# Kernel tuning notes

Hardware: AMD Instinct MI355X
Metric: run time of the kernel (lower is better)

The kernel has to match this reference:

```python
import jax, jax.numpy as jnp
import numpy as np

N = 50000
NUM_USERS = 20000
E = 800000
IN_DIM = 256
OUT_DIM = 256
H = 8
DK = OUT_DIM // H


def setup_inputs() -> dict:
    key = jax.random.key(0)
    ks = jax.random.split(key, 16)
    inp = {
        "x": jax.random.normal(ks[0], (N, IN_DIM), dtype=jnp.float32),
        "row": jax.random.randint(ks[1], (E,), 0, N, dtype=jnp.int32),
        "col": jax.random.randint(ks[2], (E,), 0, N, dtype=jnp.int32),
        "relation_emb": jax.random.normal(ks[3], (OUT_DIM,), dtype=jnp.float32),
        "user_text_embs": jax.random.normal(ks[4], (NUM_USERS, IN_DIM), dtype=jnp.float32),
        "item_text_embs": jax.random.normal(ks[5], (N - NUM_USERS, IN_DIM), dtype=jnp.float32),
        "Wq": jax.random.normal(ks[6], (OUT_DIM, IN_DIM), dtype=jnp.float32) * 0.02,
        "bq": jnp.zeros((OUT_DIM,), dtype=jnp.float32),
        "Wk": jax.random.normal(ks[7], (OUT_DIM, IN_DIM), dtype=jnp.float32) * 0.02,
        "bk": jnp.zeros((OUT_DIM,), dtype=jnp.float32),
        "Wv": jax.random.normal(ks[8], (OUT_DIM, IN_DIM), dtype=jnp.float32) * 0.02,
        "bv": jnp.zeros((OUT_DIM,), dtype=jnp.float32),
        "Wo": jax.random.normal(ks[9], (OUT_DIM, OUT_DIM), dtype=jnp.float32) * 0.02,
        "bo": jnp.zeros((OUT_DIM,), dtype=jnp.float32),
    }
    return inp


def reference(x, row, col, relation_emb, user_text_embs, item_text_embs,
              Wq, bq, Wk, bk, Wv, bv, Wo, bo):
    # text_emb: users first, then items (matches torch zeros_like + slice assign)
    text_emb = jnp.concatenate([user_text_embs, item_text_embs], axis=0)  # [N, in_dim]

    Q = (text_emb @ Wq.T + bq).reshape(N, H, DK)
    K = (text_emb @ Wk.T + bk).reshape(N, H, DK)
    V = (x @ Wv.T + bv).reshape(N, H, DK)

    Q_ = Q[col]  # [E, H, DK]
    K_ = K[row]
    V_ = V[row]
    rel = relation_emb.reshape(1, H, DK)

    scores = jnp.sum(Q_ * (K_ + rel), axis=-1) / np.sqrt(DK).astype(np.float32)  # [E, H]

    # segment softmax over destination node (col)
    m = jax.ops.segment_max(scores, col, num_segments=N)          # [N, H]
    e = jnp.exp(scores - m[col])                                   # [E, H]
    denom = jax.ops.segment_sum(e, col, num_segments=N)           # [N, H]
    attn = e / denom[col]                                          # [E, H]

    out = jax.ops.segment_sum(attn[:, :, None] * V_, col, num_segments=N)  # [N, H, DK]
    out = out.reshape(N, OUT_DIM)
    return out @ Wo.T + bo
```

## Files before the change

### kernel.cpp

```cpp
#include <hip/hip_runtime.h>
#include <hip/hip_bf16.h>

#define N_NODES   50000
#define N_USERS   20000
#define N_EDGES   800000
#define DIM       256
#define NHEAD     8
#define DKH       32
#define NBLK_SCAN ((N_NODES + 255) / 256)
#define NGRP_PAD  3128
#define NBLK_HIST ((N_EDGES + 255) / 256)
#define NBLK_G64  (NGRP_PAD / 4)
#define KVROW     768

typedef __attribute__((ext_vector_type(8))) short bf16x8;
typedef __attribute__((ext_vector_type(4))) float f32x4;
typedef __attribute__((ext_vector_type(4))) unsigned short u16x4;
typedef __attribute__((ext_vector_type(8))) unsigned short u16x8;

__device__ inline unsigned short f2bf(float f) {
    union { __hip_bfloat16 b; unsigned short u; } cv;
    cv.b = __float2bfloat16(f);
    return cv.u;
}
__device__ inline float bf2f(unsigned short u) {
    return __uint_as_float(((unsigned int)u) << 16);
}
__device__ inline unsigned char f2fp8(float f) {
    unsigned int p = __builtin_amdgcn_cvt_pk_fp8_f32(f, f, 0, false);
    return (unsigned char)(p & 0xff);
}


__global__ void prep_kernel(const float* __restrict__ Wq, const float* __restrict__ Wk,
                            const float* __restrict__ Wv, const float* __restrict__ Wo,
                            unsigned short* __restrict__ Wb2,
                            const int* __restrict__ col, int* __restrict__ cnt,
                            int* __restrict__ erank)
{
    int b = blockIdx.x;
    if (b < 128) {
        int gid = b * 256 + threadIdx.x;
        const float* srcs[4] = { Wq, Wk, Wv, Wo };
        int m = gid >> 13, slot = gid & 8191;
        int lane = slot & 63, ks = (slot >> 6) & 7, g = slot >> 9;
        int c = g * 16 + (lane & 15);
        int d = ks * 32 + (lane >> 4) * 8;
        const float* s = srcs[m] + (size_t)c * DIM + d;
        float4 f0 = *(const float4*)s, f1 = *(const float4*)(s + 4);
        u16x8 o = { f2bf(f0.x), f2bf(f0.y), f2bf(f0.z), f2bf(f0.w),
                    f2bf(f1.x), f2bf(f1.y), f2bf(f1.z), f2bf(f1.w) };
        *(u16x8*)(Wb2 + (size_t)m * 65536 + (size_t)slot * 8) = o;
    } else {
        int e = (b - 128) * 256 + threadIdx.x;
        if (e < N_EDGES) erank[e] = atomicAdd(&cnt[col[e]], 1);
    }
}

__device__ __forceinline__ void stage_a_lds(const float* __restrict__ Alo,
                                            const float* __restrict__ Ahi,
                                            int split, int row0, int M,
                                            unsigned short* Asm, int tid)
{
    const int w = tid >> 6, lane = tid & 63;
    #pragma unroll
    for (int it = 0; it < 8; ++it) {
        int f = it * 4 + w;
        int g = f >> 3, ks = f & 7;
        int r = g * 16 + (lane & 15);
        int d = ks * 32 + (lane >> 4) * 8;
        int ga = row0 + r; if (ga >= M) ga = M - 1;
        const float* src = ((ga < split) ? Alo + (size_t)ga * DIM
                                         : Ahi + (size_t)(ga - split) * DIM) + d;
        float4 f0 = *(const float4*)src, f1 = *(const float4*)(src + 4);
        u16x8 hv = { f2bf(f0.x), f2bf(f0.y), f2bf(f0.z), f2bf(f0.w),
                     f2bf(f1.x), f2bf(f1.y), f2bf(f1.z), f2bf(f1.w) };
        *(u16x8*)((char*)Asm + (size_t)f * 1024 + lane * 16) = hv;
    }
}

__device__ __forceinline__ void mfma_core_lds(const unsigned short* Asm,
                                              const unsigned short* __restrict__ W2,
                                              f32x4 acc[2][8], int lane, int wid)
{
    const int gAl = (wid >> 1) * 2;
    const int gB = (wid & 1) * 8;
    #pragma unroll
    for (int ks = 0; ks < 8; ++ks) {
        bf16x8 a[2], b[8];
        #pragma unroll
        for (int i = 0; i < 2; ++i)
            a[i] = *(const bf16x8*)((const char*)Asm + (size_t)((gAl + i) * 8 + ks) * 1024 + lane * 16);
        #pragma unroll
        for (int j = 0; j < 8; ++j)
            b[j] = *(const bf16x8*)(W2 + (size_t)((gB + j) * 8 + ks) * 512 + lane * 8);
        #pragma unroll
        for (int i = 0; i < 2; ++i)
            #pragma unroll
            for (int j = 0; j < 8; ++j)
                acc[i][j] = __builtin_amdgcn_mfma_f32_16x16x32_bf16(a[i], b[j], acc[i][j], 0, 0, 0);
    }
}

__device__ __forceinline__ void mfma_core64(const unsigned short* __restrict__ A2,
                                            const unsigned short* __restrict__ W2,
                                            int row0, f32x4 acc[2][8],
                                            int lane, int wid)
{
    const int gA = (row0 >> 4) + (wid >> 1) * 2;
    const int gB = (wid & 1) * 8;
    #pragma unroll
    for (int ks = 0; ks < 8; ++ks) {
        bf16x8 a[2], b[8];
        #pragma unroll
        for (int i = 0; i < 2; ++i)
            a[i] = *(const bf16x8*)(A2 + (size_t)((gA + i) * 8 + ks) * 512 + lane * 8);
        #pragma unroll
        for (int j = 0; j < 8; ++j)
            b[j] = *(const bf16x8*)(W2 + (size_t)((gB + j) * 8 + ks) * 512 + lane * 8);
        #pragma unroll
        for (int i = 0; i < 2; ++i)
            #pragma unroll
            for (int j = 0; j < 8; ++j)
                acc[i][j] = __builtin_amdgcn_mfma_f32_16x16x32_bf16(a[i], b[j], acc[i][j], 0, 0, 0);
    }
}

template<int MODE>
__device__ __forceinline__ void epilogue64(f32x4 acc[2][8], const float* bias, void* Cv,
                                           int row0, int M, int lane, int wid)
{
    const int wm = wid >> 1, wn = wid & 1;
    const int lr = lane & 15, lk = lane >> 4;
    float* Cf = (float*)Cv;
    unsigned short* Cb = (unsigned short*)Cv;
    unsigned char* C8 = (unsigned char*)Cv;
    #pragma unroll
    for (int i = 0; i < 2; ++i) {
        #pragma unroll
        for (int r = 0; r < 4; ++r) {
            int grow = row0 + wm * 32 + i * 16 + lk * 4 + r;
            if (grow >= M) continue;
            #pragma unroll
            for (int j = 0; j < 8; ++j) {
                int gcol = wn * 128 + j * 16 + lr;
                float val = acc[i][j][r] + bias[gcol];
                if constexpr (MODE == 0) {
                    Cf[(size_t)grow * 256 + gcol] = val;
                } else if constexpr (MODE == 1) {
                    Cb[(size_t)grow * 256 + gcol] = f2bf(val);
                } else if constexpr (MODE == 2) {
                    C8[(size_t)grow * KVROW + gcol] = f2fp8(val);
                } else {
                    *(unsigned short*)(C8 + (size_t)grow * KVROW + 256 + gcol * 2) = f2bf(val);
                }
            }
        }
    }
}

__global__ __launch_bounds__(256) void gemm_qkv_scatter(
    const float* __restrict__ user, const float* __restrict__ item,
    const float* __restrict__ x,
    const unsigned short* __restrict__ Wb2,
    const float* __restrict__ bq, const float* __restrict__ bk, const float* __restrict__ bv,
    unsigned short* __restrict__ Qb, unsigned char* __restrict__ KVb, int M,
    const int* __restrict__ row, const int* __restrict__ col,
    const int* __restrict__ erank, const int* __restrict__ offs,
    int* __restrict__ esrc)
{
    const int b = blockIdx.x;
    if (b < NBLK_HIST) {
        int e = b * 256 + threadIdx.x;
        if (e < N_EDGES) {
            int c = col[e];
            esrc[offs[c] + erank[e]] = row[e];
        }
        return;
    }
    __shared__ unsigned short Asm[64 * 256];
    const int gb = b - NBLK_HIST;
    const int isv = gb >= NBLK_G64;
    const int row0 = (isv ? gb - NBLK_G64 : gb) * 64;
    const int tid = threadIdx.x;
    const int lane = tid & 63, wid = tid >> 6;

    if (isv) stage_a_lds(x, x, M, row0, M, Asm, tid);
    else     stage_a_lds(user, item, N_USERS, row0, M, Asm, tid);
    __syncthreads();

    f32x4 acc[2][8];
    if (isv) {
        #pragma unroll
        for (int i = 0; i < 2; ++i)
            #pragma unroll
            for (int j = 0; j < 8; ++j) acc[i][j] = (f32x4){0.f, 0.f, 0.f, 0.f};
        mfma_core_lds(Asm, Wb2 + 2 * 65536, acc, lane, wid);
        epilogue64<3>(acc, bv, KVb, row0, M, lane, wid);
    } else {
        #pragma unroll
        for (int i = 0; i < 2; ++i)
            #pragma unroll
            for (int j = 0; j < 8; ++j) acc[i][j] = (f32x4){0.f, 0.f, 0.f, 0.f};
        mfma_core_lds(Asm, Wb2, acc, lane, wid);
        epilogue64<1>(acc, bq, Qb, row0, M, lane, wid);
        #pragma unroll
        for (int i = 0; i < 2; ++i)
            #pragma unroll
            for (int j = 0; j < 8; ++j) acc[i][j] = (f32x4){0.f, 0.f, 0.f, 0.f};
        mfma_core_lds(Asm, Wb2 + 65536, acc, lane, wid);
        epilogue64<2>(acc, bk, KVb, row0, M, lane, wid);
    }
}

__global__ __launch_bounds__(256) void gemm_o_reg(
    const unsigned short* __restrict__ A2,
    const unsigned short* __restrict__ Wb2, const float* __restrict__ bo,
    float* __restrict__ C, int M)
{
    const int tid = threadIdx.x;
    const int lane = tid & 63, wid = tid >> 6;
    const int row0 = blockIdx.x * 64;

    f32x4 acc[2][8];
    #pragma unroll
    for (int i = 0; i < 2; ++i)
        #pragma unroll
        for (int j = 0; j < 8; ++j) acc[i][j] = (f32x4){0.f, 0.f, 0.f, 0.f};

    mfma_core64(A2, Wb2 + 3 * 65536, row0, acc, lane, wid);
    epilogue64<0>(acc, bo, C, row0, M, lane, wid);
}

__global__ __launch_bounds__(256) void scan_blk_kernel(const int* __restrict__ cnt,
                                                       int* __restrict__ offs_tmp,
                                                       int* __restrict__ bsum) {
    __shared__ int s[256];
    int b = blockIdx.x, t = threadIdx.x;
    int i = b * 256 + t;
    int v = (i < N_NODES) ? cnt[i] : 0;
    s[t] = v;
    __syncthreads();
    #pragma unroll
    for (int d = 1; d < 256; d <<= 1) {
        int u = (t >= d) ? s[t - d] : 0;
        __syncthreads();
        s[t] += u;
        __syncthreads();
    }
    if (i < N_NODES) offs_tmp[i] = s[t] - v;
    if (t == 255) bsum[b] = s[255];
}

__global__ __launch_bounds__(256) void scan_add_kernel(const int* __restrict__ offs_tmp,
                                                       const int* __restrict__ bsum,
                                                       int* __restrict__ offs) {
    __shared__ int s[256];
    int t = threadIdx.x;
    s[t] = (t < NBLK_SCAN) ? bsum[t] : 0;
    __syncthreads();
    #pragma unroll
    for (int d = 1; d < 256; d <<= 1) {
        int u = (t >= d) ? s[t - d] : 0;
        __syncthreads();
        s[t] += u;
        __syncthreads();
    }
    int boff = (blockIdx.x == 0) ? 0 : s[blockIdx.x - 1];
    int i = blockIdx.x * 256 + t;
    if (i == 0) offs[N_NODES] = N_EDGES;
    if (i >= N_NODES) return;
    offs[i] = offs_tmp[i] + boff;
}

__global__ __launch_bounds__(256) void node_fused_kernel(
    const unsigned short* __restrict__ Qb, const unsigned char* __restrict__ KVb,
    const float* __restrict__ rel,
    const int* __restrict__ offs, const int* __restrict__ esrc,
    unsigned short* __restrict__ outagg2)
{
    const float SC = 0.17677669529663687f;
    int wid = (blockIdx.x * blockDim.x + threadIdx.x) >> 6;
    int lane = threadIdx.x & 63;
    if (wid >= N_NODES) return;
    int beg = offs[wid], end = offs[wid + 1];
    int d0 = lane * 4;
    const unsigned char* kbase = KVb + lane * 4;
    const unsigned char* vbase = KVb + 256 + lane * 8;

    u16x4 qb4 = *(const u16x4*)(Qb + (size_t)wid * DIM + d0);
    float qx = bf2f(qb4[0]), qy = bf2f(qb4[1]), qz = bf2f(qb4[2]), qw = bf2f(qb4[3]);
    float4 rl = *(const float4*)(rel + d0);

    float p0 = qx * rl.x + qy * rl.y + qz * rl.z + qw * rl.w;
    p0 += __shfl_xor(p0, 1);
    p0 += __shfl_xor(p0, 2);
    p0 += __shfl_xor(p0, 4);

    float den = 0.f;
    float4 acc = make_float4(0.f, 0.f, 0.f, 0.f);

    for (int base = beg; base < end; base += 64) {
        int n = end - base; if (n > 64) n = 64;
        int idx = base + lane; if (idx >= end) idx = end - 1;
        int my = esrc[idx];
        int j = 0;
        for (; j + 8 <= n; j += 8) {
            unsigned int kw[8]; u16x4 vv[8];
            #pragma unroll
            for (int u = 0; u < 8; ++u) {
                int r = __shfl(my, j + u);
                size_t ro = (size_t)r * KVROW;
                kw[u] = *(const unsigned int*)(kbase + ro);
                vv[u] = *(const u16x4*)(vbase + ro);
            }
            float s[8];
            #pragma unroll
            for (int u = 0; u < 8; ++u)
                s[u] = qx * __builtin_amdgcn_cvt_f32_fp8(kw[u], 0)
                     + qy * __builtin_amdgcn_cvt_f32_fp8(kw[u], 1)
                     + qz * __builtin_amdgcn_cvt_f32_fp8(kw[u], 2)
                     + qw * __builtin_amdgcn_cvt_f32_fp8(kw[u], 3);
            #pragma unroll
            for (int u = 0; u < 8; ++u) {
                s[u] += __shfl_xor(s[u], 1);
                s[u] += __shfl_xor(s[u], 2);
                s[u] += __shfl_xor(s[u], 4);
            }
            #pragma unroll
            for (int u = 0; u < 8; ++u) {
                float w = __expf((s[u] + p0) * SC);
                den += w;
                acc.x += w * bf2f(vv[u][0]); acc.y += w * bf2f(vv[u][1]);
                acc.z += w * bf2f(vv[u][2]); acc.w += w * bf2f(vv[u][3]);
            }
        }
        for (; j + 4 <= n; j += 4) {
            unsigned int kw[4]; u16x4 vv[4];
            #pragma unroll
            for (int u = 0; u < 4; ++u) {
                int r = __shfl(my, j + u);
                size_t ro = (size_t)r * KVROW;
                kw[u] = *(const unsigned int*)(kbase + ro);
                vv[u] = *(const u16x4*)(vbase + ro);
            }
            float s[4];
            #pragma unroll
            for (int u = 0; u < 4; ++u)
                s[u] = qx * __builtin_amdgcn_cvt_f32_fp8(kw[u], 0)
                     + qy * __builtin_amdgcn_cvt_f32_fp8(kw[u], 1)
                     + qz * __builtin_amdgcn_cvt_f32_fp8(kw[u], 2)
                     + qw * __builtin_amdgcn_cvt_f32_fp8(kw[u], 3);
            #pragma unroll
            for (int u = 0; u < 4; ++u) {
                s[u] += __shfl_xor(s[u], 1);
                s[u] += __shfl_xor(s[u], 2);
                s[u] += __shfl_xor(s[u], 4);
            }
            #pragma unroll
            for (int u = 0; u < 4; ++u) {
                float w = __expf((s[u] + p0) * SC);
                den += w;
                acc.x += w * bf2f(vv[u][0]); acc.y += w * bf2f(vv[u][1]);
                acc.z += w * bf2f(vv[u][2]); acc.w += w * bf2f(vv[u][3]);
            }
        }
        for (; j < n; ++j) {
            int r = __shfl(my, j);
            size_t ro = (size_t)r * KVROW;
            unsigned int kw = *(const unsigned int*)(kbase + ro);
            u16x4 vv = *(const u16x4*)(vbase + ro);
            float s0 = qx * __builtin_amdgcn_cvt_f32_fp8(kw, 0)
                     + qy * __builtin_amdgcn_cvt_f32_fp8(kw, 1)
                     + qz * __builtin_amdgcn_cvt_f32_fp8(kw, 2)
                     + qw * __builtin_amdgcn_cvt_f32_fp8(kw, 3);
            s0 += __shfl_xor(s0, 1);
            s0 += __shfl_xor(s0, 2);
            s0 += __shfl_xor(s0, 4);
            float w0 = __expf((s0 + p0) * SC);
            den += w0;
            acc.x += w0 * bf2f(vv[0]); acc.y += w0 * bf2f(vv[1]);
            acc.z += w0 * bf2f(vv[2]); acc.w += w0 * bf2f(vv[3]);
        }
    }
    float rden = (end > beg) ? 1.f / den : 0.f;
    u16x4 o = { f2bf(acc.x * rden), f2bf(acc.y * rden),
                f2bf(acc.z * rden), f2bf(acc.w * rden) };
    int ks = lane >> 3, lk = (lane >> 1) & 3, e4 = (lane & 1) * 4;
    size_t toff = ((size_t)(wid >> 4) * 8 + ks) * 512 + (lk * 16 + (wid & 15)) * 8 + e4;
    *(u16x4*)(outagg2 + toff) = o;
}

extern "C" void kernel_launch(void* const* d_in, const int* in_sizes, int n_in,
                              void* d_out, int out_size, void* d_ws, size_t ws_size,
                              hipStream_t stream) {
    const float* x    = (const float*)d_in[0];
    const int*   row  = (const int*)d_in[1];
    const int*   col  = (const int*)d_in[2];
    const float* rel  = (const float*)d_in[3];
    const float* user = (const float*)d_in[4];
    const float* item = (const float*)d_in[5];
    const float* Wq   = (const float*)d_in[6];
    const float* bq   = (const float*)d_in[7];
    const float* Wk   = (const float*)d_in[8];
    const float* bk   = (const float*)d_in[9];
    const float* Wv   = (const float*)d_in[10];
    const float* bv   = (const float*)d_in[11];
    const float* Wo   = (const float*)d_in[12];
    const float* bo   = (const float*)d_in[13];

    char* ws = (char*)d_ws;
    size_t off = 0;
    auto alloc = [&](size_t bytes) -> void* {
        void* p = ws + off;
        off = (off + bytes + 255) & ~(size_t)255;
        return p;
    };
    const size_t tiled_sz = (size_t)NGRP_PAD * 4096 * 2;
    unsigned short* Qb      = (unsigned short*)alloc((size_t)N_NODES * DIM * 2);
    unsigned char*  KVb     = (unsigned char*)alloc((size_t)N_NODES * KVROW);
    unsigned short* outagg2 = (unsigned short*)alloc(tiled_sz);
    unsigned short* Wb2     = (unsigned short*)alloc((size_t)4 * 65536 * 2);
    int*   cnt      = (int*)alloc((size_t)N_NODES * 4);
    int*   offs     = (int*)alloc((size_t)(N_NODES + 1) * 4);
    int*   offs_tmp = (int*)alloc((size_t)N_NODES * 4);
    int*   bsum     = (int*)alloc((size_t)NBLK_SCAN * 4);
    int*   esrc     = (int*)alloc((size_t)N_EDGES * 4);
    int*   erank    = (int*)alloc((size_t)N_EDGES * 4);

    hipMemsetAsync(cnt, 0, (size_t)N_NODES * 4, stream);

    prep_kernel<<<128 + NBLK_HIST, 256, 0, stream>>>(
        Wq, Wk, Wv, Wo, Wb2, col, cnt, erank);
    scan_blk_kernel<<<NBLK_SCAN, 256, 0, stream>>>(cnt, offs_tmp, bsum);
    scan_add_kernel<<<NBLK_SCAN, 256, 0, stream>>>(offs_tmp, bsum, offs);

    gemm_qkv_scatter<<<NBLK_HIST + 2 * NBLK_G64, 256, 0, stream>>>(
        user, item, x, Wb2, bq, bk, bv, Qb, KVb, N_NODES,
        row, col, erank, offs, esrc);

    node_fused_kernel<<<(N_NODES * 64 + 255) / 256, 256, 0, stream>>>(
        Qb, KVb, rel, offs, esrc, outagg2);

    gemm_o_reg<<<NBLK_G64, 256, 0, stream>>>(outagg2, Wb2, bo, (float*)d_out, N_NODES);
}
```

Before: 230.9 us.

## Split QKV GEMM A-tile staging into halves to overlap global loads with MFMA

The QKV projection kernel now stages its 64-row A tile in two 32-row halves. It loads the second half into registers while the MFMAs and epilogue for the first half run, then writes that half to LDS behind a second barrier. This is meant to hide global-load latency behind compute in a kernel that previously loaded the whole tile before doing any math. The cost is extra registers for the prefetch buffer, a second __syncthreads, and weight B-fragments that are now reloaded for each half, which may reduce occupancy.

```diff
diff --git a/kernel.cpp b/kernel.cpp
--- a/kernel.cpp
+++ b/kernel.cpp
@@ -57,48 +57,55 @@
     }
 }
 
-__device__ __forceinline__ void stage_a_lds(const float* __restrict__ Alo,
-                                            const float* __restrict__ Ahi,
-                                            int split, int row0, int M,
-                                            unsigned short* Asm, int tid)
+__device__ __forceinline__ void load_half(const float* __restrict__ Alo,
+                                          const float* __restrict__ Ahi,
+                                          int split, int row0, int M, int h,
+                                          int tid, float4 (&rg)[4][2])
 {
     const int w = tid >> 6, lane = tid & 63;
     #pragma unroll
-    for (int it = 0; it < 8; ++it) {
-        int f = it * 4 + w;
+    for (int it = 0; it < 4; ++it) {
+        int f = h * 16 + it * 4 + w;
         int g = f >> 3, ks = f & 7;
         int r = g * 16 + (lane & 15);
         int d = ks * 32 + (lane >> 4) * 8;
         int ga = row0 + r; if (ga >= M) ga = M - 1;
         const float* src = ((ga < split) ? Alo + (size_t)ga * DIM
                                          : Ahi + (size_t)(ga - split) * DIM) + d;
-        float4 f0 = *(const float4*)src, f1 = *(const float4*)(src + 4);
-        u16x8 hv = { f2bf(f0.x), f2bf(f0.y), f2bf(f0.z), f2bf(f0.w),
-                     f2bf(f1.x), f2bf(f1.y), f2bf(f1.z), f2bf(f1.w) };
+        rg[it][0] = *(const float4*)src;
+        rg[it][1] = *(const float4*)(src + 4);
+    }
+}
+
+__device__ __forceinline__ void write_half(unsigned short* Asm, int h, int tid,
+                                           const float4 (&rg)[4][2])
+{
+    const int w = tid >> 6, lane = tid & 63;
+    #pragma unroll
+    for (int it = 0; it < 4; ++it) {
+        int f = h * 16 + it * 4 + w;
+        u16x8 hv = { f2bf(rg[it][0].x), f2bf(rg[it][0].y), f2bf(rg[it][0].z), f2bf(rg[it][0].w),
+                     f2bf(rg[it][1].x), f2bf(rg[it][1].y), f2bf(rg[it][1].z), f2bf(rg[it][1].w) };
         *(u16x8*)((char*)Asm + (size_t)f * 1024 + lane * 16) = hv;
     }
 }
 
-__device__ __forceinline__ void mfma_core_lds(const unsigned short* Asm,
-                                              const unsigned short* __restrict__ W2,
-                                              f32x4 acc[2][8], int lane, int wid)
-{
-    const int gAl = (wid >> 1) * 2;
+__device__ __forceinline__ void mfma_half(const unsigned short* Asm,
+                                          const unsigned short* __restrict__ W2,
+                                          int h, f32x4 acc[8], int lane, int wid)
+{
+    const int gA = h * 2 + (wid >> 1);
     const int gB = (wid & 1) * 8;
     #pragma unroll
     for (int ks = 0; ks < 8; ++ks) {
-        bf16x8 a[2], b[8];
-        #pragma unroll
-        for (int i = 0; i < 2; ++i)
-            a[i] = *(const bf16x8*)((const char*)Asm + (size_t)((gAl + i) * 8 + ks) * 1024 + lane * 16);
+        bf16x8 a = *(const bf16x8*)((const char*)Asm + (size_t)(gA * 8 + ks) * 1024 + lane * 16);
+        bf16x8 b[8];
         #pragma unroll
         for (int j = 0; j < 8; ++j)
             b[j] = *(const bf16x8*)(W2 + (size_t)((gB + j) * 8 + ks) * 512 + lane * 8);
         #pragma unroll
-        for (int i = 0; i < 2; ++i)
-            #pragma unroll
-            for (int j = 0; j < 8; ++j)
-                acc[i][j] = __builtin_amdgcn_mfma_f32_16x16x32_bf16(a[i], b[j], acc[i][j], 0, 0, 0);
+        for (int j = 0; j < 8; ++j)
+            acc[j] = __builtin_amdgcn_mfma_f32_16x16x32_bf16(a, b[j], acc[j], 0, 0, 0);
     }
 }
 
@@ -127,14 +134,37 @@
 }
 
 template<int MODE>
-__device__ __forceinline__ void epilogue64(f32x4 acc[2][8], const float* bias, void* Cv,
-                                           int row0, int M, int lane, int wid)
+__device__ __forceinline__ void epi_half(f32x4 acc[8], const float* bias, void* Cv,
+                                         int row0, int h, int M, int lane, int wid)
 {
     const int wm = wid >> 1, wn = wid & 1;
     const int lr = lane & 15, lk = lane >> 4;
-    float* Cf = (float*)Cv;
     unsigned short* Cb = (unsigned short*)Cv;
     unsigned char* C8 = (unsigned char*)Cv;
+    #pragma unroll
+    for (int r = 0; r < 4; ++r) {
+        int grow = row0 + h * 32 + wm * 16 + lk * 4 + r;
+        if (grow >= M) continue;
+        #pragma unroll
+        for (int j = 0; j < 8; ++j) {
+            int gcol = wn * 128 + j * 16 + lr;
+            float val = acc[j][r] + bias[gcol];
+            if constexpr (MODE == 1) {
+                Cb[(size_t)grow * 256 + gcol] = f2bf(val);
+            } else if constexpr (MODE == 2) {
+                C8[(size_t)grow * KVROW + gcol] = f2fp8(val);
+            } else {
+                *(unsigned short*)(C8 + (size_t)grow * KVROW + 256 + gcol * 2) = f2bf(val);
+            }
+        }
+    }
+}
+
+__device__ __forceinline__ void epilogue_f32(f32x4 acc[2][8], const float* bias, float* Cf,
+                                             int row0, int M, int lane, int wid)
+{
+    const int wm = wid >> 1, wn = wid & 1;
+    const int lr = lane & 15, lk = lane >> 4;
     #pragma unroll
     for (int i = 0; i < 2; ++i) {
         #pragma unroll
@@ -144,16 +174,7 @@
             #pragma unroll
             for (int j = 0; j < 8; ++j) {
                 int gcol = wn * 128 + j * 16 + lr;
-                float val = acc[i][j][r] + bias[gcol];
-                if constexpr (MODE == 0) {
-                    Cf[(size_t)grow * 256 + gcol] = val;
-                } else if constexpr (MODE == 1) {
-                    Cb[(size_t)grow * 256 + gcol] = f2bf(val);
-                } else if constexpr (MODE == 2) {
-                    C8[(size_t)grow * KVROW + gcol] = f2fp8(val);
-                } else {
-                    *(unsigned short*)(C8 + (size_t)grow * KVROW + 256 + gcol * 2) = f2bf(val);
-                }
+                Cf[(size_t)grow * 256 + gcol] = acc[i][j][r] + bias[gcol];
             }
         }
     }
@@ -185,31 +206,49 @@
     const int tid = threadIdx.x;
     const int lane = tid & 63, wid = tid >> 6;
 
-    if (isv) stage_a_lds(x, x, M, row0, M, Asm, tid);
-    else     stage_a_lds(user, item, N_USERS, row0, M, Asm, tid);
+    const float* Alo = isv ? x : user;
+    const float* Ahi = isv ? x : item;
+    const int split  = isv ? M : N_USERS;
+
+    float4 rg0[4][2], rg1[4][2];
+    load_half(Alo, Ahi, split, row0, M, 0, tid, rg0);
+    write_half(Asm, 0, tid, rg0);
     __syncthreads();
 
-    f32x4 acc[2][8];
+    load_half(Alo, Ahi, split, row0, M, 1, tid, rg1);
+
     if (isv) {
-        #pragma unroll
-        for (int i = 0; i < 2; ++i)
-            #pragma unroll
-            for (int j = 0; j < 8; ++j) acc[i][j] = (f32x4){0.f, 0.f, 0.f, 0.f};
-        mfma_core_lds(Asm, Wb2 + 2 * 65536, acc, lane, wid);
-        epilogue64<3>(acc, bv, KVb, row0, M, lane, wid);
+        f32x4 av[8];
+        #pragma unroll
+        for (int j = 0; j < 8; ++j) av[j] = (f32x4){0.f, 0.f, 0.f, 0.f};
+        mfma_half(Asm, Wb2 + 2 * 65536, 0, av, lane, wid);
+        epi_half<3>(av, bv, KVb, row0, 0, M, lane, wid);
+
+        write_half(Asm, 1, tid, rg1);
+        __syncthreads();
+
+        #pragma unroll
+        for (int j = 0; j < 8; ++j) av[j] = (f32x4){0.f, 0.f, 0.f, 0.f};
+        mfma_half(Asm, Wb2 + 2 * 65536, 1, av, lane, wid);
+        epi_half<3>(av, bv, KVb, row0, 1, M, lane, wid);
     } else {
-        #pragma unroll
-        for (int i = 0; i < 2; ++i)
-            #pragma unroll
-            for (int j = 0; j < 8; ++j) acc[i][j] = (f32x4){0.f, 0.f, 0.f, 0.f};
-        mfma_core_lds(Asm, Wb2, acc, lane, wid);
-        epilogue64<1>(acc, bq, Qb, row0, M, lane, wid);
-        #pragma unroll
-        for (int i = 0; i < 2; ++i)
-            #pragma unroll
-            for (int j = 0; j < 8; ++j) acc[i][j] = (f32x4){0.f, 0.f, 0.f, 0.f};
-        mfma_core_lds(Asm, Wb2 + 65536, acc, lane, wid);
-        epilogue64<2>(acc, bk, KVb, row0, M, lane, wid);
+        f32x4 aq[8], ak[8];
+        #pragma unroll
+        for (int j = 0; j < 8; ++j) { aq[j] = (f32x4){0.f, 0.f, 0.f, 0.f}; ak[j] = (f32x4){0.f, 0.f, 0.f, 0.f}; }
+        mfma_half(Asm, Wb2, 0, aq, lane, wid);
+        mfma_half(Asm, Wb2 + 65536, 0, ak, lane, wid);
+        epi_half<1>(aq, bq, Qb, row0, 0, M, lane, wid);
+        epi_half<2>(ak, bk, KVb, row0, 0, M, lane, wid);
+
+        write_half(Asm, 1, tid, rg1);
+        __syncthreads();
+
+        #pragma unroll
+        for (int j = 0; j < 8; ++j) { aq[j] = (f32x4){0.f, 0.f, 0.f, 0.f}; ak[j] = (f32x4){0.f, 0.f, 0.f, 0.f}; }
+        mfma_half(Asm, Wb2, 1, aq, lane, wid);
+        mfma_half(Asm, Wb2 + 65536, 1, ak, lane, wid);
+        epi_half<1>(aq, bq, Qb, row0, 1, M, lane, wid);
+        epi_half<2>(ak, bk, KVb, row0, 1, M, lane, wid);
     }
 }
 
@@ -229,7 +268,7 @@
         for (int j = 0; j < 8; ++j) acc[i][j] = (f32x4){0.f, 0.f, 0.f, 0.f};
 
     mfma_core64(A2, Wb2 + 3 * 65536, row0, acc, lane, wid);
-    epilogue64<0>(acc, bo, C, row0, M, lane, wid);
+    epilogue_f32(acc, bo, C, row0, M, lane, wid);
 }
 
 __global__ __launch_bounds__(256) void scan_blk_kernel(const int* __restrict__ cnt,
```

New measurement: 294.4 us. +27.5%, slower.
